# Kernel tuning notes

Measured on AMD Instinct MI355X. Metric: run time of the kernel, lower is better.

The kernel has to match this reference:

```python
import jax, jax.numpy as jnp
import numpy as np

B, P, K = 128, 1024, 4  # 128 clouds of 1024 points, kNN k=4 (includes self, as PyG knn does)


def _edge_mlp(e, W1, b1, W2, b2):
    # PyG MLP([2d, c, c]) with plain_last=True: ReLU after first linear only;
    # batch-norm at init (running_mean=0, var=1) is identity in eval mode.
    h = jax.nn.relu(e @ W1 + b1)
    return h @ W2 + b2


def _dynamic_edge_conv(x, W1, b1, W2, b2):
    # x: [B, P, d]. Recompute kNN graph in feature space per cloud, build edge
    # features [x_i, x_j - x_i], apply MLP, max-aggregate over neighbors.
    sq = jnp.sum(x * x, axis=-1)  # [B,P]
    dist = sq[:, :, None] + sq[:, None, :] - 2.0 * jnp.einsum('bid,bjd->bij', x, x)  # [B,P,P]
    _, idx = jax.lax.top_k(-dist, K)  # [B,P,K] nearest neighbors (self included, dist 0)
    xj = jax.vmap(lambda xc, ic: xc[ic])(x, idx)  # [B,P,K,d]
    xi = jnp.broadcast_to(x[:, :, None, :], xj.shape)
    e = jnp.concatenate([xi, xj - xi], axis=-1)  # [B,P,K,2d]
    h = _edge_mlp(e, W1, b1, W2, b2)  # [B,P,K,c]
    return jnp.max(h, axis=2)  # max aggregation -> [B,P,c]


def setup_inputs() -> dict:
    key = jax.random.key(0)
    ks = jax.random.split(key, 24)
    s = 0.1
    d = {
        'x': jax.random.normal(ks[0], (B * P, 1), dtype=jnp.float32),
        'batch': (jnp.arange(B * P, dtype=jnp.int32) // P),
        # conv1: MLP([2, 32, 32])
        'c1W1': s * jax.random.normal(ks[1], (2, 32)), 'c1b1': jnp.zeros((32,)),
        'c1W2': s * jax.random.normal(ks[2], (32, 32)), 'c1b2': jnp.zeros((32,)),
        # conv2: MLP([64, 32, 32])
        'c2W1': s * jax.random.normal(ks[3], (64, 32)), 'c2b1': jnp.zeros((32,)),
        'c2W2': s * jax.random.normal(ks[4], (32, 32)), 'c2b2': jnp.zeros((32,)),
        # conv3: MLP([64, 64, 64])
        'c3W1': s * jax.random.normal(ks[5], (64, 64)), 'c3b1': jnp.zeros((64,)),
        'c3W2': s * jax.random.normal(ks[6], (64, 64)), 'c3b2': jnp.zeros((64,)),
        # final MLP([128, 264, 264, 264, 2]), norm=None, dropout inactive in eval
        'mW1': s * jax.random.normal(ks[7], (128, 264)), 'mb1': jnp.zeros((264,)),
        'mW2': s * jax.random.normal(ks[8], (264, 264)), 'mb2': jnp.zeros((264,)),
        'mW3': s * jax.random.normal(ks[9], (264, 264)), 'mb3': jnp.zeros((264,)),
        'mW4': s * jax.random.normal(ks[10], (264, 2)), 'mb4': jnp.zeros((2,)),
    }
    return d


def reference(x, batch, c1W1, c1b1, c1W2, c1b2, c2W1, c2b1, c2W2, c2b2,
              c3W1, c3b1, c3W2, c3b2, mW1, mb1, mW2, mb2, mW3, mb3, mW4, mb4):
    # batch ids are contiguous equal-size groups (arange // P); use reshape.
    xb = x.reshape(B, P, -1)
    x1 = _dynamic_edge_conv(xb, c1W1, c1b1, c1W2, c1b2)  # [B,P,32]
    x2 = _dynamic_edge_conv(x1, c2W1, c2b1, c2W2, c2b2)  # [B,P,32]
    x3 = _dynamic_edge_conv(x2, c3W1, c3b1, c3W2, c3b2)  # [B,P,64]
    f = jnp.concatenate([x1, x2, x3], axis=-1).reshape(B * P, -1)  # [N,128]
    h = jax.nn.relu(f @ mW1 + mb1)
    h = jax.nn.relu(h @ mW2 + mb2)
    h = jax.nn.relu(h @ mW3 + mb3)
    out = h @ mW4 + mb4  # [N,2]
    return jax.nn.log_softmax(out, axis=1)
```

## Files before the change

### kernel.cpp

```cpp
#include <hip/hip_runtime.h>
#include <hip/hip_bf16.h>
#include <float.h>
#include <math.h>

#define BB 128
#define PP 1024
#define KNN 4
#define NROWS (BB * PP)

typedef __bf16 v8bf __attribute__((ext_vector_type(8)));
typedef float  v4f  __attribute__((ext_vector_type(4)));

__device__ inline unsigned short f2bs(float f) {
    __hip_bfloat16 h = __float2bfloat16(f);
    return *(unsigned short*)&h;
}
__device__ inline unsigned packbf2(float a, float b) {
    return (unsigned)f2bs(a) | ((unsigned)f2bs(b) << 16);
}
__device__ inline float bflo(unsigned u) { return __builtin_bit_cast(float, u << 16); }
__device__ inline float bfhi(unsigned u) { return __builtin_bit_cast(float, u & 0xFFFF0000u); }

__device__ inline unsigned med3u(unsigned a, unsigned b, unsigned c) {
    unsigned d;
    asm("v_med3_u32 %0, %1, %2, %3" : "=v"(d) : "v"(a), "v"(b), "v"(c));
    return d;
}

__global__ __launch_bounds__(256)
void pack_kernel(const float* __restrict__ src, int D,
                 __hip_bfloat16* __restrict__ xh, __hip_bfloat16* __restrict__ xl,
                 float* __restrict__ sq)
{
    const int t = blockIdx.x * 256 + threadIdx.x;
    const int row = t >> 2, part = t & 3;
    float v[8];
    #pragma unroll
    for (int u = 0; u < 8; u++) {
        int d = part * 8 + u;
        v[u] = (d < D) ? src[(size_t)row * D + d] : 0.f;
    }
    float s = 0.f;
    unsigned int hw[4], lw[4];
    #pragma unroll
    for (int w = 0; w < 4; w++) {
        unsigned short h2[2], l2[2];
        #pragma unroll
        for (int e = 0; e < 2; e++) {
            float x = v[2 * w + e];
            __hip_bfloat16 hb = __float2bfloat16(x);
            float hf = __bfloat162float(hb);
            __hip_bfloat16 lb = __float2bfloat16(x - hf);
            h2[e] = *(unsigned short*)&hb;
            l2[e] = *(unsigned short*)&lb;
            s = fmaf(x, x, s);
        }
        hw[w] = (unsigned int)h2[0] | ((unsigned int)h2[1] << 16);
        lw[w] = (unsigned int)l2[0] | ((unsigned int)l2[1] << 16);
    }
    s += __shfl_xor(s, 1);
    s += __shfl_xor(s, 2);
    uint4 hv; hv.x = hw[0]; hv.y = hw[1]; hv.z = hw[2]; hv.w = hw[3];
    uint4 lv; lv.x = lw[0]; lv.y = lw[1]; lv.z = lw[2]; lv.w = lw[3];
    *(uint4*)&xh[(size_t)row * 32 + part * 8] = hv;
    *(uint4*)&xl[(size_t)row * 32 + part * 8] = lv;
    if (part == 0) sq[row] = s;
}

__global__ __launch_bounds__(256, 4)
void knn_mfma(const __hip_bfloat16* __restrict__ xh, const __hip_bfloat16* __restrict__ xl,
              const float* __restrict__ sq, int* __restrict__ nidx)
{
    __shared__ __align__(16) char scb[64 * 256];
    unsigned* cand = (unsigned*)scb;

    const int tid = threadIdx.x;
    const int wv = tid >> 6, lane = tid & 63;
    const int lr = lane & 15, lq = lane >> 4;
    const int b = blockIdx.y, i0 = blockIdx.x * 64;
    const size_t Rb = (size_t)b * PP;

    v8bf ah[4], al[4];
    #pragma unroll
    for (int it = 0; it < 4; it++) {
        size_t g = Rb + i0 + it * 16 + lr;
        ah[it] = __builtin_bit_cast(v8bf, *(const uint4*)(xh + g * 32 + lq * 8));
        al[it] = __builtin_bit_cast(v8bf, *(const uint4*)(xl + g * 32 + lq * 8));
    }

    float sqq[4][4];
    #pragma unroll
    for (int it = 0; it < 4; it++)
        #pragma unroll
        for (int m = 0; m < 4; m++)
            sqq[it][m] = sq[Rb + i0 + it * 16 + lq * 4 + m];

    const int r = tid & 63, qt = tid >> 6;
    unsigned m0 = ~0u, m1 = ~0u, m2 = ~0u, m3 = ~0u;

    for (int ch = 0; ch < 8; ch++) {
        #pragma unroll
        for (int jt2 = 0; jt2 < 2; jt2++) {
            const int tl = wv * 2 + jt2;
            const size_t gj = Rb + ch * 128 + tl * 16 + lr;
            v8bf bh = __builtin_bit_cast(v8bf, *(const uint4*)(xh + gj * 32 + lq * 8));
            v8bf bl = __builtin_bit_cast(v8bf, *(const uint4*)(xl + gj * 32 + lq * 8));
            const float sqv = sq[gj];
            const unsigned jloc = (unsigned)(ch * 128 + tl * 16 + lr);
            const int cb = wv * 64 + lr * 4;
            #pragma unroll
            for (int it = 0; it < 4; it++) {
                v4f a = (v4f){0.f, 0.f, 0.f, 0.f};
                a = __builtin_amdgcn_mfma_f32_16x16x32_bf16(al[it], bl, a, 0, 0, 0);
                a = __builtin_amdgcn_mfma_f32_16x16x32_bf16(al[it], bh, a, 0, 0, 0);
                a = __builtin_amdgcn_mfma_f32_16x16x32_bf16(ah[it], bl, a, 0, 0, 0);
                a = __builtin_amdgcn_mfma_f32_16x16x32_bf16(ah[it], bh, a, 0, 0, 0);
                #pragma unroll
                for (int m = 0; m < 4; m++) {
                    float s = fmaf(-2.f, a[m], sqv + sqq[it][m]);
                    s = fmaxf(s, 0.f);
                    unsigned key = (__builtin_bit_cast(unsigned, s) & 0xFFFFFC00u) | jloc;
                    const int row = it * 16 + lq * 4 + m;
                    *(unsigned*)(scb + row * 256 + (cb ^ ((row & 7) << 4))) = key;
                }
            }
            __asm__ volatile("" ::: "memory");
            {
                const int rsw = (r & 7) << 4;
                #pragma unroll
                for (int s4 = 0; s4 < 4; s4++) {
                    uint4 kv = *(const uint4*)(scb + r * 256 + ((qt * 64 + s4 * 16) ^ rsw));
                    unsigned kk[4] = {kv.x, kv.y, kv.z, kv.w};
                    #pragma unroll
                    for (int e = 0; e < 4; e++) {
                        unsigned k = kk[e];
                        unsigned n0 = min(m0, k);
                        unsigned n1 = med3u(m0, m1, k);
                        unsigned n2 = med3u(m1, m2, k);
                        unsigned n3 = med3u(m2, m3, k);
                        m0 = n0; m1 = n1; m2 = n2; m3 = n3;
                    }
                }
            }
            __asm__ volatile("" ::: "memory");
        }
    }

    __syncthreads();
    cand[(qt * 4 + 0) * 64 + r] = m0;
    cand[(qt * 4 + 1) * 64 + r] = m1;
    cand[(qt * 4 + 2) * 64 + r] = m2;
    cand[(qt * 4 + 3) * 64 + r] = m3;
    __syncthreads();

    if (tid < 64) {
        unsigned g0 = ~0u, g1 = ~0u, g2 = ~0u, g3 = ~0u;
        #pragma unroll
        for (int s2 = 0; s2 < 16; s2++) {
            unsigned k = cand[s2 * 64 + tid];
            unsigned n0 = min(g0, k);
            unsigned n1 = med3u(g0, g1, k);
            unsigned n2 = med3u(g1, g2, k);
            unsigned n3 = med3u(g2, g3, k);
            g0 = n0; g1 = n1; g2 = n2; g3 = n3;
        }
        const int base = (int)Rb;
        int* op = nidx + (size_t)(Rb + i0 + tid) * KNN;
        op[0] = base + (int)(g0 & 1023u);
        op[1] = base + (int)(g1 & 1023u);
        op[2] = base + (int)(g2 & 1023u);
        op[3] = base + (int)(g3 & 1023u);
    }
}

template<int D, int H, int C, typename OT>
__global__ __launch_bounds__(256, 4)
void edge_mfma(const float* __restrict__ x, const int* __restrict__ nidx,
               const __hip_bfloat16* __restrict__ EW1, const __hip_bfloat16* __restrict__ EW2,
               const float* __restrict__ b1g, const float* __restrict__ b2g,
               OT* __restrict__ out)
{
    constexpr int NE = 256;
    constexpr int TDP = (D == 1) ? 32 : 64;
    constexpr int DP  = TDP / 2;
    constexpr int P   = ((TDP > H) ? TDP : H) + 8;
    constexpr int NT1 = H / 16, NT2 = C / 16;
    constexpr int KS1 = TDP / 32, KS2 = H / 32;

    __shared__ __hip_bfloat16 xe[NE * P];

    const int tid = threadIdx.x;
    const int wv = tid >> 6, lane = tid & 63;
    const int lr = lane & 15, q = lane >> 4;
    const int p0 = blockIdx.x * 64;

    {
        const int e = wv * 64 + lane;
        const int j = nidx[(size_t)p0 * KNN + e];
        const int pi = p0 + (e >> 2);
        if constexpr (D == 1) {
            #pragma unroll
            for (int s = 0; s < P / 8; s++) {
                uint4 z; z.x = 0u; z.y = 0u; z.z = 0u; z.w = 0u;
                *(uint4*)&xe[e * P + s * 8] = z;
            }
            xe[e * P + 0]  = __float2bfloat16(x[pi]);
            xe[e * P + DP] = __float2bfloat16(x[j]);
        } else {
            const float* si = x + (size_t)pi * D;
            const float* sj = x + (size_t)j * D;
            #pragma unroll
            for (int s = 0; s < D / 8; s++) {
                float4 f0 = *(const float4*)&si[s * 8];
                float4 f1 = *(const float4*)&si[s * 8 + 4];
                uint4 uv;
                uv.x = packbf2(f0.x, f0.y); uv.y = packbf2(f0.z, f0.w);
                uv.z = packbf2(f1.x, f1.y); uv.w = packbf2(f1.z, f1.w);
                *(uint4*)&xe[e * P + s * 8] = uv;
            }
            #pragma unroll
            for (int s = 0; s < D / 8; s++) {
                float4 f0 = *(const float4*)&sj[s * 8];
                float4 f1 = *(const float4*)&sj[s * 8 + 4];
                uint4 uv;
                uv.x = packbf2(f0.x, f0.y); uv.y = packbf2(f0.z, f0.w);
                uv.z = packbf2(f1.x, f1.y); uv.w = packbf2(f1.z, f1.w);
                *(uint4*)&xe[e * P + DP + s * 8] = uv;
            }
        }
    }

    v4f acc1[4][NT1];
    #pragma unroll
    for (int mi = 0; mi < 4; mi++)
        #pragma unroll
        for (int nt = 0; nt < NT1; nt++) acc1[mi][nt] = (v4f){0.f, 0.f, 0.f, 0.f};

    #pragma unroll
    for (int ks = 0; ks < KS1; ks++) {
        v8bf a[4];
        #pragma unroll
        for (int mi = 0; mi < 4; mi++)
            a[mi] = __builtin_bit_cast(v8bf,
                *(const uint4*)&xe[(wv * 64 + mi * 16 + lr) * P + ks * 32 + q * 8]);
        v8bf b[NT1];
        #pragma unroll
        for (int nt = 0; nt < NT1; nt++)
            b[nt] = __builtin_bit_cast(v8bf,
                *(const uint4*)(EW1 + (size_t)(nt * 16 + lr) * TDP + ks * 32 + q * 8));
        #pragma unroll
        for (int mi = 0; mi < 4; mi++)
            #pragma unroll
            for (int nt = 0; nt < NT1; nt++)
                acc1[mi][nt] = __builtin_amdgcn_mfma_f32_16x16x32_bf16(a[mi], b[nt], acc1[mi][nt], 0, 0, 0);
    }
    #pragma unroll
    for (int nt = 0; nt < NT1; nt++) {
        const float bias = b1g[nt * 16 + lr];
        #pragma unroll
        for (int mi = 0; mi < 4; mi++) {
            #pragma unroll
            for (int m = 0; m < 4; m++) {
                int row = wv * 64 + mi * 16 + q * 4 + m;
                xe[row * P + nt * 16 + lr] =
                    __float2bfloat16(fmaxf(acc1[mi][nt][m] + bias, 0.f));
            }
        }
    }

    v4f acc2[4][NT2];
    #pragma unroll
    for (int mi = 0; mi < 4; mi++)
        #pragma unroll
        for (int nt = 0; nt < NT2; nt++) acc2[mi][nt] = (v4f){0.f, 0.f, 0.f, 0.f};

    #pragma unroll
    for (int ks = 0; ks < KS2; ks++) {
        v8bf a[4];
        #pragma unroll
        for (int mi = 0; mi < 4; mi++)
            a[mi] = __builtin_bit_cast(v8bf,
                *(const uint4*)&xe[(wv * 64 + mi * 16 + lr) * P + ks * 32 + q * 8]);
        v8bf b[NT2];
        #pragma unroll
        for (int nt = 0; nt < NT2; nt++)
            b[nt] = __builtin_bit_cast(v8bf,
                *(const uint4*)(EW2 + (size_t)(nt * 16 + lr) * H + ks * 32 + q * 8));
        #pragma unroll
        for (int mi = 0; mi < 4; mi++)
            #pragma unroll
            for (int nt = 0; nt < NT2; nt++)
                acc2[mi][nt] = __builtin_amdgcn_mfma_f32_16x16x32_bf16(a[mi], b[nt], acc2[mi][nt], 0, 0, 0);
    }
    #pragma unroll
    for (int nt = 0; nt < NT2; nt++) {
        const int c = nt * 16 + lr;
        const float bias = b2g[c];
        #pragma unroll
        for (int mi = 0; mi < 4; mi++) {
            float v = fmaxf(fmaxf(acc2[mi][nt][0], acc2[mi][nt][1]),
                            fmaxf(acc2[mi][nt][2], acc2[mi][nt][3])) + bias;
            const int p = p0 + (wv * 4 + mi) * 4 + q;
            if constexpr (sizeof(OT) == 4) out[(size_t)p * C + c] = v;
            else                           out[(size_t)p * C + c] = __float2bfloat16(v);
        }
    }
}

__global__ void prep_kernel(const float* __restrict__ mW1, const float* __restrict__ mW2,
                            const float* __restrict__ mW3,
                            const float* __restrict__ mb1, const float* __restrict__ mb2,
                            const float* __restrict__ mb3,
                            const float* __restrict__ c1W1, const float* __restrict__ c1W2,
                            const float* __restrict__ c2W1, const float* __restrict__ c2W2,
                            const float* __restrict__ c3W1, const float* __restrict__ c3W2,
                            __hip_bfloat16* __restrict__ WT1, __hip_bfloat16* __restrict__ WT2,
                            __hip_bfloat16* __restrict__ WT3, float* __restrict__ bp,
                            __hip_bfloat16* __restrict__ E11, __hip_bfloat16* __restrict__ E12,
                            __hip_bfloat16* __restrict__ E13,
                            __hip_bfloat16* __restrict__ E21, __hip_bfloat16* __restrict__ E22,
                            __hip_bfloat16* __restrict__ E23)
{
    const int t0 = blockIdx.x * blockDim.x + threadIdx.x;
    const int NT = gridDim.x * blockDim.x;
    for (int i = t0; i < 272 * 136; i += NT) {
        int n = i / 136, k = i - n * 136;
        WT1[i] = (n < 264 && k < 128) ? __float2bfloat16(mW1[(size_t)k * 264 + n]) : __float2bfloat16(0.f);
    }
    for (int i = t0; i < 272 * 296; i += NT) {
        int n = i / 296, k = i - n * 296;
        WT2[i] = (n < 264 && k < 264) ? __float2bfloat16(mW2[(size_t)k * 264 + n]) : __float2bfloat16(0.f);
        WT3[i] = (n < 264 && k < 264) ? __float2bfloat16(mW3[(size_t)k * 264 + n]) : __float2bfloat16(0.f);
    }
    for (int i = t0; i < 3 * 272; i += NT) {
        int l = i / 272, n = i - l * 272;
        const float* bsrc = (l == 0) ? mb1 : (l == 1) ? mb2 : mb3;
        bp[i] = (n < 264) ? bsrc[n] : 0.f;
    }
    for (int i = t0; i < 32 * 32; i += NT) {
        int h = i >> 5, k = i & 31;
        float v = (k == 0) ? (c1W1[h] - c1W1[32 + h]) : (k == 16 ? c1W1[32 + h] : 0.f);
        E11[i] = __float2bfloat16(v);
    }
    for (int i = t0; i < 32 * 64; i += NT) {
        int h = i >> 6, k = i & 63;
        float v = (k < 32) ? (c2W1[k * 32 + h] - c2W1[(k + 32) * 32 + h]) : c2W1[k * 32 + h];
        E12[i] = __float2bfloat16(v);
    }
    for (int i = t0; i < 64 * 64; i += NT) {
        int h = i >> 6, k = i & 63;
        float v = (k < 32) ? (c3W1[k * 64 + h] - c3W1[(k + 32) * 64 + h]) : c3W1[k * 64 + h];
        E13[i] = __float2bfloat16(v);
    }
    for (int i = t0; i < 32 * 32; i += NT) {
        int c = i >> 5, h = i & 31;
        E21[i] = __float2bfloat16(c1W2[h * 32 + c]);
        E22[i] = __float2bfloat16(c2W2[h * 32 + c]);
    }
    for (int i = t0; i < 64 * 64; i += NT) {
        int c = i >> 6, h = i & 63;
        E23[i] = __float2bfloat16(c3W2[h * 64 + c]);
    }
}

#define ACT_RB 640

template<int NK>
__device__ __forceinline__ void mlp_layer(
    char* actb, const __hip_bfloat16* __restrict__ WT, const int KP,
    const float* __restrict__ bias, const int wv, const int rlane, const int ph)
{
    v4f acc[2][4], acc16;
    #pragma unroll
    for (int i = 0; i < 2; i++)
        #pragma unroll
        for (int rt = 0; rt < 4; rt++) acc[i][rt] = (v4f){0.f, 0.f, 0.f, 0.f};
    acc16 = (v4f){0.f, 0.f, 0.f, 0.f};

    const int sw = (rlane & 7) << 4;
    const __hip_bfloat16* wbase = WT + (size_t)rlane * KP + ph * 8;
    const bool has16 = (wv >= 4);
    const int r16 = ((wv - 4) & 3) * 16 + rlane;

    v8bf wb[2][2], wb16[2];
    auto loadW = [&](int ks, int buf) {
        wb[buf][0] = __builtin_bit_cast(v8bf,
            *(const uint4*)(wbase + (size_t)wv * 16 * KP + ks * 32));
        wb[buf][1] = __builtin_bit_cast(v8bf,
            *(const uint4*)(wbase + (size_t)(8 + wv) * 16 * KP + ks * 32));
        if (has16)
            wb16[buf] = __builtin_bit_cast(v8bf,
                *(const uint4*)(wbase + (size_t)256 * KP + ks * 32));
    };
    loadW(0, 0);

    #pragma unroll
    for (int ks = 0; ks < NK; ks++) {
        const int cur = ks & 1;
        if (ks + 1 < NK) loadW(ks + 1, cur ^ 1);
        v8bf ab[4], ab16;
        #pragma unroll
        for (int rt = 0; rt < 4; rt++)
            ab[rt] = __builtin_bit_cast(v8bf,
                *(const uint4*)(actb + (rt * 16 + rlane) * ACT_RB + ((ks * 64 + ph * 16) ^ sw)));
        if (has16)
            ab16 = __builtin_bit_cast(v8bf,
                *(const uint4*)(actb + r16 * ACT_RB + ((ks * 64 + ph * 16) ^ sw)));
        #pragma unroll
        for (int i = 0; i < 2; i++)
            #pragma unroll
            for (int rt = 0; rt < 4; rt++)
                acc[i][rt] = __builtin_amdgcn_mfma_f32_16x16x32_bf16(wb[cur][i], ab[rt], acc[i][rt], 0, 0, 0);
        if (has16)
            acc16 = __builtin_amdgcn_mfma_f32_16x16x32_bf16(wb16[cur], ab16, acc16, 0, 0, 0);
    }
    __syncthreads();

    #pragma unroll
    for (int i = 0; i < 2; i++) {
        const int col0 = (wv + 8 * i) * 16 + ph * 4;
        const float4 bv = *(const float4*)&bias[col0];
        #pragma unroll
        for (int rt = 0; rt < 4; rt++) {
            const int row = rt * 16 + rlane;
            ushort4 pk;
            pk.x = f2bs(fmaxf(acc[i][rt][0] + bv.x, 0.f));
            pk.y = f2bs(fmaxf(acc[i][rt][1] + bv.y, 0.f));
            pk.z = f2bs(fmaxf(acc[i][rt][2] + bv.z, 0.f));
            pk.w = f2bs(fmaxf(acc[i][rt][3] + bv.w, 0.f));
            *(ushort4*)(actb + row * ACT_RB + ((col0 * 2) ^ ((rlane & 7) << 4))) = pk;
        }
    }
    if (has16) {
        const int col0 = 256 + ph * 4;
        const float4 bv = *(const float4*)&bias[col0];
        ushort4 pk;
        pk.x = f2bs(fmaxf(acc16[0] + bv.x, 0.f));
        pk.y = f2bs(fmaxf(acc16[1] + bv.y, 0.f));
        pk.z = f2bs(fmaxf(acc16[2] + bv.z, 0.f));
        pk.w = f2bs(fmaxf(acc16[3] + bv.w, 0.f));
        *(ushort4*)(actb + r16 * ACT_RB + ((col0 * 2) ^ ((rlane & 7) << 4))) = pk;
    }
    __syncthreads();
}

__global__ __launch_bounds__(512, 4)
void mlp_kernel(const float* __restrict__ x1, const float* __restrict__ x2,
                const __hip_bfloat16* __restrict__ x3,
                const __hip_bfloat16* __restrict__ WT1, const __hip_bfloat16* __restrict__ WT2,
                const __hip_bfloat16* __restrict__ WT3, const float* __restrict__ bp,
                const float* __restrict__ mW4, const float* __restrict__ mb4,
                float* __restrict__ outp)
{
    __shared__ __align__(16) char actb[64 * ACT_RB];
    __shared__ __align__(16) float W4s[264 * 2 + 2];
    __shared__ float lsm[512];

    const int tid = threadIdx.x;
    const int wv = tid >> 6, lane = tid & 63;
    const int rlane = lane & 15, ph = lane >> 4;
    const size_t row0 = (size_t)blockIdx.x * 64;

    {
        uint4 z; z.x = 0u; z.y = 0u; z.z = 0u; z.w = 0u;
        for (int t = tid; t < 64 * 6; t += 512) {
            int r = t / 6, s = t - r * 6;
            int cb = (34 + s) * 16;
            *(uint4*)(actb + r * ACT_RB + (cb ^ ((r & 7) << 4))) = z;
        }
        for (int t = tid; t < 64 * 8; t += 512) {
            int r = t >> 3, g = t & 7;
            size_t grow = row0 + r;
            const int swr = (r & 7) << 4;
            float4 fa = *(const float4*)&x1[grow * 32 + g * 4];
            uint2 ua; ua.x = packbf2(fa.x, fa.y); ua.y = packbf2(fa.z, fa.w);
            *(uint2*)(actb + r * ACT_RB + ((g * 8) ^ swr)) = ua;
            float4 fb = *(const float4*)&x2[grow * 32 + g * 4];
            uint2 ub; ub.x = packbf2(fb.x, fb.y); ub.y = packbf2(fb.z, fb.w);
            *(uint2*)(actb + r * ACT_RB + ((64 + g * 8) ^ swr)) = ub;
            uint4 uc = *(const uint4*)&x3[grow * 64 + g * 8];
            *(uint4*)(actb + r * ACT_RB + ((128 + g * 16) ^ swr)) = uc;
        }
        for (int t = tid; t < 530; t += 512) {
            if (t < 528) { int c = t / 264, k2 = t - c * 264; W4s[t] = mW4[(size_t)k2 * 2 + c]; }
            else W4s[t] = mb4[t - 528];
        }
    }
    __syncthreads();

    mlp_layer<4>(actb, WT1, 136, bp,       wv, rlane, ph);
    mlp_layer<9>(actb, WT2, 296, bp + 272, wv, rlane, ph);
    mlp_layer<9>(actb, WT3, 296, bp + 544, wv, rlane, ph);

    {
        const int r = tid >> 3, rem = tid & 7;
        const int c = rem >> 2, h = rem & 3;
        const float* wp = &W4s[c * 264];
        const int swr = (r & 7) << 4;
        const int k0 = (h == 0) ? 0 : (8 + 64 * h);
        const int k1 = k0 + ((h == 0) ? 72 : 64);
        float s = 0.f;
        for (int k = k0; k < k1; k += 8) {
            uint4 u = *(const uint4*)(actb + r * ACT_RB + ((2 * k) ^ swr));
            float4 wa = *(const float4*)&wp[k];
            float4 wb2 = *(const float4*)&wp[k + 4];
            s = fmaf(bflo(u.x), wa.x, s); s = fmaf(bfhi(u.x), wa.y, s);
            s = fmaf(bflo(u.y), wa.z, s); s = fmaf(bfhi(u.y), wa.w, s);
            s = fmaf(bflo(u.z), wb2.x, s); s = fmaf(bfhi(u.z), wb2.y, s);
            s = fmaf(bflo(u.w), wb2.z, s); s = fmaf(bfhi(u.w), wb2.w, s);
        }
        lsm[tid] = s;
    }
    __syncthreads();
    if (tid < 64) {
        float l0 = lsm[tid * 8 + 0] + lsm[tid * 8 + 1] + lsm[tid * 8 + 2] + lsm[tid * 8 + 3] + W4s[528];
        float l1 = lsm[tid * 8 + 4] + lsm[tid * 8 + 5] + lsm[tid * 8 + 6] + lsm[tid * 8 + 7] + W4s[529];
        float m = fmaxf(l0, l1);
        float lse = m + __logf(__expf(l0 - m) + __expf(l1 - m));
        float2 o; o.x = l0 - lse; o.y = l1 - lse;
        *(float2*)&outp[(row0 + tid) * 2] = o;
    }
}

extern "C" void kernel_launch(void* const* d_in, const int* in_sizes, int n_in,
                              void* d_out, int out_size, void* d_ws, size_t ws_size,
                              hipStream_t stream)
{
    const float* x    = (const float*)d_in[0];
    const float* c1W1 = (const float*)d_in[2];
    const float* c1b1 = (const float*)d_in[3];
    const float* c1W2 = (const float*)d_in[4];
    const float* c1b2 = (const float*)d_in[5];
    const float* c2W1 = (const float*)d_in[6];
    const float* c2b1 = (const float*)d_in[7];
    const float* c2W2 = (const float*)d_in[8];
    const float* c2b2 = (const float*)d_in[9];
    const float* c3W1 = (const float*)d_in[10];
    const float* c3b1 = (const float*)d_in[11];
    const float* c3W2 = (const float*)d_in[12];
    const float* c3b2 = (const float*)d_in[13];
    const float* mW1  = (const float*)d_in[14];
    const float* mb1  = (const float*)d_in[15];
    const float* mW2  = (const float*)d_in[16];
    const float* mb2  = (const float*)d_in[17];
    const float* mW3  = (const float*)d_in[18];
    const float* mb3  = (const float*)d_in[19];
    const float* mW4  = (const float*)d_in[20];
    const float* mb4  = (const float*)d_in[21];

    float* x1 = (float*)d_ws;
    float* x2 = x1 + (size_t)NROWS * 32;
    __hip_bfloat16* x3 = (__hip_bfloat16*)(x2 + (size_t)NROWS * 32);
    int* nidx = (int*)(x3 + (size_t)NROWS * 64);
    __hip_bfloat16* WT1 = (__hip_bfloat16*)(nidx + (size_t)NROWS * 4);
    __hip_bfloat16* WT2 = WT1 + 272 * 136;
    __hip_bfloat16* WT3 = WT2 + 272 * 296;
    float* bp = (float*)(WT3 + 272 * 296);
    __hip_bfloat16* xph = (__hip_bfloat16*)(bp + 3 * 272);
    __hip_bfloat16* xpl = xph + (size_t)NROWS * 32;
    float* sqw = (float*)(xpl + (size_t)NROWS * 32);
    __hip_bfloat16* E11 = (__hip_bfloat16*)(sqw + NROWS);
    __hip_bfloat16* E12 = E11 + 32 * 32;
    __hip_bfloat16* E13 = E12 + 32 * 64;
    __hip_bfloat16* E21 = E13 + 64 * 64;
    __hip_bfloat16* E22 = E21 + 32 * 32;
    __hip_bfloat16* E23 = E22 + 32 * 32;

    prep_kernel<<<dim3(512), 256, 0, stream>>>(mW1, mW2, mW3, mb1, mb2, mb3,
                                               c1W1, c1W2, c2W1, c2W2, c3W1, c3W2,
                                               WT1, WT2, WT3, bp,
                                               E11, E12, E13, E21, E22, E23);

    dim3 kgrid(PP / 64, BB);
    dim3 pgrid(NROWS * 4 / 256);
    dim3 egrid(NROWS / 64);

    pack_kernel<<<pgrid, 256, 0, stream>>>(x, 1, xph, xpl, sqw);
    knn_mfma<<<kgrid, 256, 0, stream>>>(xph, xpl, sqw, nidx);
    edge_mfma<1, 32, 32, float><<<egrid, 256, 0, stream>>>(x, nidx, E11, E21, c1b1, c1b2, x1);

    pack_kernel<<<pgrid, 256, 0, stream>>>(x1, 32, xph, xpl, sqw);
    knn_mfma<<<kgrid, 256, 0, stream>>>(xph, xpl, sqw, nidx);
    edge_mfma<32, 32, 32, float><<<egrid, 256, 0, stream>>>(x1, nidx, E12, E22, c2b1, c2b2, x2);

    pack_kernel<<<pgrid, 256, 0, stream>>>(x2, 32, xph, xpl, sqw);
    knn_mfma<<<kgrid, 256, 0, stream>>>(xph, xpl, sqw, nidx);
    edge_mfma<32, 64, 64, __hip_bfloat16><<<egrid, 256, 0, stream>>>(x2, nidx, E13, E23, c3b1, c3b2, x3);

    mlp_kernel<<<dim3(NROWS / 64), 512, 0, stream>>>(x1, x2, x3, WT1, WT2, WT3, bp,
                                                     mW4, mb4, (float*)d_out);
}
```

Before: 409.7 us.

## Fuse kNN feature packing into edge-conv epilogue and deepen MLP weight prefetch

The edge-conv kernel now writes the hi/lo bf16 split of its output and the per-point squared norm directly from its epilogue, so two separate pack_kernel launches and their re-reads of x1/x2 disappear. The squared norm is reduced across lanes with shuffles. Separately, the MLP layer's weight prefetch moves from double to triple buffering, loading two k-steps ahead. This raises register pressure and adds scattered 2-byte stores to the edge kernel.

```diff
diff --git a/kernel.cpp b/kernel.cpp
--- a/kernel.cpp
+++ b/kernel.cpp
@@ -173,12 +173,14 @@
     }
 }
 
-template<int D, int H, int C, typename OT>
+template<int D, int H, int C, typename OT, bool PACK>
 __global__ __launch_bounds__(256, 4)
 void edge_mfma(const float* __restrict__ x, const int* __restrict__ nidx,
                const __hip_bfloat16* __restrict__ EW1, const __hip_bfloat16* __restrict__ EW2,
                const float* __restrict__ b1g, const float* __restrict__ b2g,
-               OT* __restrict__ out)
+               OT* __restrict__ out,
+               __hip_bfloat16* __restrict__ xhw, __hip_bfloat16* __restrict__ xlw,
+               float* __restrict__ sqw)
 {
     constexpr int NE = 256;
     constexpr int TDP = (D == 1) ? 32 : 64;
@@ -293,16 +295,35 @@
                 acc2[mi][nt] = __builtin_amdgcn_mfma_f32_16x16x32_bf16(a[mi], b[nt], acc2[mi][nt], 0, 0, 0);
     }
     #pragma unroll
-    for (int nt = 0; nt < NT2; nt++) {
-        const int c = nt * 16 + lr;
-        const float bias = b2g[c];
-        #pragma unroll
-        for (int mi = 0; mi < 4; mi++) {
+    for (int mi = 0; mi < 4; mi++) {
+        const int p = p0 + (wv * 4 + mi) * 4 + q;
+        float vs[NT2];
+        float ss = 0.f;
+        #pragma unroll
+        for (int nt = 0; nt < NT2; nt++) {
+            const int c = nt * 16 + lr;
             float v = fmaxf(fmaxf(acc2[mi][nt][0], acc2[mi][nt][1]),
-                            fmaxf(acc2[mi][nt][2], acc2[mi][nt][3])) + bias;
-            const int p = p0 + (wv * 4 + mi) * 4 + q;
+                            fmaxf(acc2[mi][nt][2], acc2[mi][nt][3])) + b2g[c];
+            vs[nt] = v;
             if constexpr (sizeof(OT) == 4) out[(size_t)p * C + c] = v;
             else                           out[(size_t)p * C + c] = __float2bfloat16(v);
+            if constexpr (PACK) ss = fmaf(v, v, ss);
+        }
+        if constexpr (PACK) {
+            ss += __shfl_xor(ss, 1);
+            ss += __shfl_xor(ss, 2);
+            ss += __shfl_xor(ss, 4);
+            ss += __shfl_xor(ss, 8);
+            #pragma unroll
+            for (int nt = 0; nt < NT2; nt++) {
+                float v = vs[nt];
+                __hip_bfloat16 hb = __float2bfloat16(v);
+                float hf = __bfloat162float(hb);
+                __hip_bfloat16 lb = __float2bfloat16(v - hf);
+                xhw[(size_t)p * 32 + nt * 16 + lr] = hb;
+                xlw[(size_t)p * 32 + nt * 16 + lr] = lb;
+            }
+            if (lr == 0) sqw[p] = ss;
         }
     }
 }
@@ -382,7 +403,7 @@
     const bool has16 = (wv >= 4);
     const int r16 = ((wv - 4) & 3) * 16 + rlane;
 
-    v8bf wb[2][2], wb16[2];
+    v8bf wb[3][2], wb16[3];
     auto loadW = [&](int ks, int buf) {
         wb[buf][0] = __builtin_bit_cast(v8bf,
             *(const uint4*)(wbase + (size_t)wv * 16 * KP + ks * 32));
@@ -393,11 +414,12 @@
                 *(const uint4*)(wbase + (size_t)256 * KP + ks * 32));
     };
     loadW(0, 0);
+    loadW(1, 1);
 
     #pragma unroll
     for (int ks = 0; ks < NK; ks++) {
-        const int cur = ks & 1;
-        if (ks + 1 < NK) loadW(ks + 1, cur ^ 1);
+        const int cur = ks % 3;
+        if (ks + 2 < NK) loadW(ks + 2, (ks + 2) % 3);
         v8bf ab[4], ab16;
         #pragma unroll
         for (int rt = 0; rt < 4; rt++)
@@ -577,15 +599,16 @@
 
     pack_kernel<<<pgrid, 256, 0, stream>>>(x, 1, xph, xpl, sqw);
     knn_mfma<<<kgrid, 256, 0, stream>>>(xph, xpl, sqw, nidx);
-    edge_mfma<1, 32, 32, float><<<egrid, 256, 0, stream>>>(x, nidx, E11, E21, c1b1, c1b2, x1);
-
-    pack_kernel<<<pgrid, 256, 0, stream>>>(x1, 32, xph, xpl, sqw);
+    edge_mfma<1, 32, 32, float, true><<<egrid, 256, 0, stream>>>(
+        x, nidx, E11, E21, c1b1, c1b2, x1, xph, xpl, sqw);
+
     knn_mfma<<<kgrid, 256, 0, stream>>>(xph, xpl, sqw, nidx);
-    edge_mfma<32, 32, 32, float><<<egrid, 256, 0, stream>>>(x1, nidx, E12, E22, c2b1, c2b2, x2);
-
-    pack_kernel<<<pgrid, 256, 0, stream>>>(x2, 32, xph, xpl, sqw);
+    edge_mfma<32, 32, 32, float, true><<<egrid, 256, 0, stream>>>(
+        x1, nidx, E12, E22, c2b1, c2b2, x2, xph, xpl, sqw);
+
     knn_mfma<<<kgrid, 256, 0, stream>>>(xph, xpl, sqw, nidx);
-    edge_mfma<32, 64, 64, __hip_bfloat16><<<egrid, 256, 0, stream>>>(x2, nidx, E13, E23, c3b1, c3b2, x3);
+    edge_mfma<32, 64, 64, __hip_bfloat16, false><<<egrid, 256, 0, stream>>>(
+        x2, nidx, E13, E23, c3b1, c3b2, x3, nullptr, nullptr, nullptr);
 
     mlp_kernel<<<dim3(NROWS / 64), 512, 0, stream>>>(x1, x2, x3, WT1, WT2, WT3, bp,
                                                      mW4, mb4, (float*)d_out);
```

After: 397.6 us. 2.9% less time.
